# Optimization experiments

Hardware: AMD Instinct MI355X
Metric: run time of the kernel (lower is better)

## Reference

```python
import jax, jax.numpy as jnp
import numpy as np

S, LC = 8192, 16
CE = CH = 64      # char embed == char hidden (original quirk)
WE, HW = 128, 256 # word embed, word hidden
WV, CV, TAGS = 50000, 128, 50


def _lstm_step(h, c, x, Wih, Whh, bih, bhh):
    # PyTorch LSTM gate order: i, f, g, o
    g = x @ Wih.T + h @ Whh.T + bih + bhh
    i, f, gg, o = jnp.split(g, 4, axis=-1)
    c = jax.nn.sigmoid(f) * c + jax.nn.sigmoid(i) * jnp.tanh(gg)
    h = jax.nn.sigmoid(o) * jnp.tanh(c)
    return h, c


def setup_inputs() -> dict:
    key = jax.random.key(0)
    ks = jax.random.split(key, 16)
    inp = {
        'word_idxs': jax.random.randint(ks[0], (S,), 0, WV),
        'char_idxs': jax.random.randint(ks[1], (S, LC), 0, CV),
        'char_lens': jax.random.randint(ks[2], (S,), 1, LC + 1),
        'char_emb': jax.random.normal(ks[3], (CV, CE), jnp.float32) * 0.1,
        'char_Wih': jax.random.normal(ks[4], (4 * CH, CE), jnp.float32) * 0.1,
        'char_Whh': jax.random.normal(ks[5], (4 * CH, CH), jnp.float32) * 0.1,
        'char_bih': jax.random.normal(ks[6], (4 * CH,), jnp.float32) * 0.1,
        'char_bhh': jax.random.normal(ks[7], (4 * CH,), jnp.float32) * 0.1,
        'word_emb': jax.random.normal(ks[8], (WV, WE), jnp.float32) * 0.1,
        'word_Wih': jax.random.normal(ks[9], (4 * HW, WE + CH), jnp.float32) * 0.1,
        'word_Whh': jax.random.normal(ks[10], (4 * HW, HW), jnp.float32) * 0.1,
        'word_bih': jax.random.normal(ks[11], (4 * HW,), jnp.float32) * 0.1,
        'word_bhh': jax.random.normal(ks[12], (4 * HW,), jnp.float32) * 0.1,
        'tag_W': jax.random.normal(ks[13], (TAGS, HW), jnp.float32) * 0.1,
        'tag_b': jax.random.normal(ks[14], (TAGS,), jnp.float32) * 0.1,
    }
    return inp


def reference(word_idxs, char_idxs, char_lens,
              char_emb, char_Wih, char_Whh, char_bih, char_bhh,
              word_emb, word_Wih, word_Whh, word_bih, word_bhh,
              tag_W, tag_b):
    # --- char LSTM over all words in parallel (one fused scan over char time) ---
    cx = char_emb[char_idxs]                      # [S, LC, CE]
    cx = jnp.transpose(cx, (1, 0, 2))             # [LC, S, CE]

    def cstep(carry, x_t):
        h, c = carry
        h, c = _lstm_step(h, c, x_t, char_Wih, char_Whh, char_bih, char_bhh)
        return (h, c), h

    h0 = jnp.zeros((S, CH), cx.dtype)
    (_, _), hs = jax.lax.scan(cstep, (h0, h0), cx)  # hs: [LC, S, CH]
    # original takes char_lstm_out[-1] == hidden at position len(chars)-1
    char_feat = hs[char_lens - 1, jnp.arange(S)]    # [S, CH]

    # --- word LSTM over the sentence (batch = 1) ---
    wx = jnp.concatenate([word_emb[word_idxs], char_feat], axis=-1)  # [S, WE+CH]

    def wstep(carry, x_t):
        h, c = carry
        h, c = _lstm_step(h, c, x_t, word_Wih, word_Whh, word_bih, word_bhh)
        return (h, c), h

    wh0 = jnp.zeros((HW,), wx.dtype)
    (_, _), outs = jax.lax.scan(wstep, (wh0, wh0), wx)  # [S, HW]

    logits = outs @ tag_W.T + tag_b                     # [S, TAGS]
    return jax.nn.log_softmax(logits, axis=-1)
```

## Files before the change

### kernel.cpp

```cpp
#include <hip/hip_runtime.h>
#include <hip/hip_bf16.h>

#define S_LEN 8192
#define LC 16
#define CE 64
#define CH 64
#define WE 128
#define NTAGS 50

using bf16 = __hip_bfloat16;
typedef unsigned int u32;
typedef unsigned long long u64;

__device__ __forceinline__ float bfbits2f(unsigned short u) {
    union { unsigned int i; float f; } v; v.i = ((unsigned int)u) << 16; return v.f;
}
__device__ __forceinline__ float sigm(float x) {
    return __builtin_amdgcn_rcpf(1.0f + __expf(-x));
}
__device__ __forceinline__ float tanh_fast(float x) {
    return 1.0f - 2.0f * __builtin_amdgcn_rcpf(__expf(2.0f * x) + 1.0f);
}

template <bool BF>
__device__ __forceinline__ float ld1(const void* p, size_t i) {
    if constexpr (BF) return bfbits2f(((const unsigned short*)p)[i]);
    else              return ((const float*)p)[i];
}
template <bool BF>
__device__ __forceinline__ float4 ld4(const void* p, size_t i) {
    if constexpr (BF) {
        const ushort4 s = *reinterpret_cast<const ushort4*>((const unsigned short*)p + i);
        return make_float4(bfbits2f(s.x), bfbits2f(s.y), bfbits2f(s.z), bfbits2f(s.w));
    } else {
        return *reinterpret_cast<const float4*>((const float*)p + i);
    }
}
template <bool BF>
__device__ __forceinline__ void st1(void* p, size_t i, float v) {
    if constexpr (BF) ((bf16*)p)[i] = __float2bfloat16(v);
    else              ((float*)p)[i] = v;
}

__global__ void kdetect(const void* emb, u32* flag) {
    const int j = threadIdx.x;
    int s = 0;
    #pragma unroll
    for (int k = 0; k < 4; ++k) {
        const unsigned short u = ((const unsigned short*)emb)[j * 4 + k];
        const int e = (u >> 7) & 0xFF;
        s += (e >= 100 && e <= 133) ? 1 : 0;
    }
    #pragma unroll
    for (int off = 32; off >= 1; off >>= 1) s += __shfl_xor(s, off, 64);
    if (j == 0) *flag = (s >= 200) ? 1u : 0u;
}

template <bool BF>
__global__ __launch_bounds__(256, 2) void kchar(
        const u32* __restrict__ dtf,
        const int* __restrict__ char_idxs, const int* __restrict__ char_lens,
        const void* __restrict__ char_emb,
        const void* __restrict__ Wih, const void* __restrict__ Whh,
        const void* __restrict__ bih, const void* __restrict__ bhh,
        float* __restrict__ cfeat) {
    if ((*dtf != 0u) != BF) return;
    const int j = threadIdx.x;
    const int w0 = blockIdx.x * 8;

    __shared__ __align__(16) float emb_lds[128 * CE];
    __shared__ __align__(16) float gates_lds[8 * 256];
    __shared__ __align__(16) float h_lds[8 * CH];
    __shared__ __align__(16) float c_lds[8 * CH];
    __shared__ int cidx_lds[8 * LC];
    __shared__ int len_lds[8];

    {
        float4* emb4 = reinterpret_cast<float4*>(emb_lds);
        #pragma unroll
        for (int i = 0; i < 8; ++i) {
            const int c = i * 256 + j;
            emb4[c] = ld4<BF>(char_emb, (size_t)c * 4);
        }
    }
    if (j < 128) cidx_lds[j] = char_idxs[w0 * LC + j];
    if (j < 8)   len_lds[j]  = char_lens[w0 + j];
    h_lds[j] = 0.f; h_lds[j + 256] = 0.f;
    c_lds[j] = 0.f; c_lds[j + 256] = 0.f;

    float4 wih4[16], whh4[16];
    #pragma unroll
    for (int kc = 0; kc < 16; ++kc) {
        wih4[kc] = ld4<BF>(Wih, (size_t)j * CE + kc * 4);
        whh4[kc] = ld4<BF>(Whh, (size_t)j * CH + kc * 4);
    }
    const float bias = ld1<BF>(bih, j) + ld1<BF>(bhh, j);
    __syncthreads();

    for (int t = 0; t < LC; ++t) {
        for (int w = 0; w < 8; ++w) {
            const int ci = cidx_lds[w * LC + t];
            const float4* x4  = reinterpret_cast<const float4*>(emb_lds + ci * CE);
            const float4* hh4 = reinterpret_cast<const float4*>(h_lds + w * CH);
            float a0 = 0.f, a1 = 0.f, a2 = 0.f, a3 = 0.f;
            #pragma unroll
            for (int kc = 0; kc < 16; ++kc) {
                const float4 xv = x4[kc]; const float4 hv = hh4[kc];
                const float4 wi = wih4[kc]; const float4 wh = whh4[kc];
                a0 = fmaf(wi.x, xv.x, a0); a1 = fmaf(wi.y, xv.y, a1);
                a2 = fmaf(wi.z, xv.z, a2); a3 = fmaf(wi.w, xv.w, a3);
                a0 = fmaf(wh.x, hv.x, a0); a1 = fmaf(wh.y, hv.y, a1);
                a2 = fmaf(wh.z, hv.z, a2); a3 = fmaf(wh.w, hv.w, a3);
            }
            gates_lds[w * 256 + j] = bias + ((a0 + a1) + (a2 + a3));
        }
        __syncthreads();
        #pragma unroll
        for (int rep = 0; rep < 2; ++rep) {
            const int p = j + rep * 256;
            const int w = p >> 6, u = p & 63;
            const float ig = gates_lds[w * 256 + u];
            const float fg = gates_lds[w * 256 + 64 + u];
            const float gg = gates_lds[w * 256 + 128 + u];
            const float og = gates_lds[w * 256 + 192 + u];
            const float cn = sigm(fg) * c_lds[p] + sigm(ig) * tanh_fast(gg);
            const float hn = sigm(og) * tanh_fast(cn);
            c_lds[p] = cn; h_lds[p] = hn;
            if (t == len_lds[w] - 1)
                cfeat[(size_t)(w0 + w) * CH + u] = hn;
        }
        __syncthreads();
    }
}

template <bool BF>
__global__ __launch_bounds__(256) void kgx(
        const u32* __restrict__ dtf,
        int t0, const int* __restrict__ word_idxs, const float* __restrict__ cfeat,
        const void* __restrict__ wemb, const void* __restrict__ Wih,
        const void* __restrict__ bih, const void* __restrict__ bhh,
        float* __restrict__ Gxr) {
    if ((*dtf != 0u) != BF) return;
    const int j = threadIdx.x;
    const int wr0 = blockIdx.x * 16;
    const int w0g = t0 + wr0;
    __shared__ __align__(16) float wx[16 * 192];
    __shared__ int widx[16];
    if (j < 16) widx[j] = word_idxs[w0g + j];
    __syncthreads();
    {
        const int w = j >> 4, ch = j & 15;
        const size_t eb = (size_t)widx[w] * WE + ch * 8;
        const float4 f0 = ld4<BF>(wemb, eb), f1 = ld4<BF>(wemb, eb + 4);
        float4* dst = reinterpret_cast<float4*>(wx + w * 192 + ch * 8);
        dst[0] = f0; dst[1] = f1;
        const float4 cf = *reinterpret_cast<const float4*>(
            cfeat + (size_t)(w0g + w) * CH + ch * 4);
        *reinterpret_cast<float4*>(wx + w * 192 + WE + ch * 4) = cf;
    }
    __syncthreads();

    for (int g = 0; g < 4; ++g) {
        const int r = g * 256 + j;
        float acc[16];
        #pragma unroll
        for (int w = 0; w < 16; ++w) acc[w] = 0.f;
        #pragma unroll 8
        for (int kc = 0; kc < 48; ++kc) {
            const float4 wv = ld4<BF>(Wih, (size_t)r * 192 + kc * 4);
            #pragma unroll
            for (int w = 0; w < 16; ++w) {
                const float4 xv = *reinterpret_cast<const float4*>(wx + w * 192 + kc * 4);
                acc[w] = fmaf(wv.x, xv.x, acc[w]);
                acc[w] = fmaf(wv.y, xv.y, acc[w]);
                acc[w] = fmaf(wv.z, xv.z, acc[w]);
                acc[w] = fmaf(wv.w, xv.w, acc[w]);
            }
        }
        const float bias = ld1<BF>(bih, r) + ld1<BF>(bhh, r);
        #pragma unroll
        for (int w = 0; w < 16; ++w)
            Gxr[(size_t)(wr0 + w) * 1024 + r] = acc[w] + bias;
    }
}

template <bool BF>
__global__ __launch_bounds__(1024, 4) void kwlstm(
        const u32* __restrict__ dtf,
        int t0, int t1, int epoch, const void* __restrict__ whh,
        const float* __restrict__ Gxr,
        float* __restrict__ hallr, u64* hgx2, float* csave, u32* xccpub) {
    if ((*dtf != 0u) != BF) return;
    const int j = threadIdx.x;

    __shared__ int role_s;
    const u32 etag = 0xB0u + ((u32)epoch & 0xFu);
    if (j == 0) {
        const u32 xcc = __builtin_amdgcn_s_getreg(6164) & 0xFu;
        __hip_atomic_store(&xccpub[blockIdx.x], (etag << 24) | xcc,
                           __ATOMIC_RELAXED, __HIP_MEMORY_SCOPE_AGENT);
    }
    if (j < 64) {
        u32 v;
        do {
            v = __hip_atomic_load(&xccpub[j], __ATOMIC_RELAXED,
                                  __HIP_MEMORY_SCOPE_AGENT);
        } while ((v >> 24) != etag);
        const u32 v0 = __shfl(v, 0, 64);
        const u64 mask = __ballot((v & 0xFu) == (v0 & 0xFu));
        const int myb = blockIdx.x;
        int role = -1;
        if (__popcll(mask) >= 4) {
            if ((mask >> myb) & 1ull) {
                const int rank = __popcll(mask & ((1ull << myb) - 1ull));
                if (rank < 4) role = rank;
            }
        } else {
            if (myb < 4) role = myb;
        }
        if (j == 0) role_s = role;
    }
    __syncthreads();
    const int b = role_s;
    if (b < 0) return;

    const int r  = j & 255;
    const int kq = j >> 8;
    const int R  = ((r >> 6) << 8) + b * 64 + (r & 63);

    __shared__ __align__(16) float h_cur[256];
    __shared__ __align__(16) float part[1024];

    float4 wv[16];
    #pragma unroll
    for (int kc = 0; kc < 16; ++kc)
        wv[kc] = ld4<BF>(whh, (size_t)R * 256 + kq * 64 + kc * 4);

    if (j < 256) h_cur[j] = 0.f;
    float c_reg = 0.f;
    if (t0 > 0 && j < 64) c_reg = csave[b * 64 + j];

    float gxA = (j < 256) ? Gxr[(size_t)0 * 1024 + R] : 0.f;
    float gxB = (j < 256 && t0 + 1 < t1) ? Gxr[(size_t)1 * 1024 + R] : 0.f;
    __syncthreads();

    for (int t = t0; t < t1; ++t) {
        if (t > 0) {
            if (t == t0) {
                if (j < 256) {
                    u64 pk;
                    do {
                        pk = __hip_atomic_load(&hgx2[(size_t)(t & 1) * 256 + j],
                                               __ATOMIC_RELAXED, __HIP_MEMORY_SCOPE_AGENT);
                    } while ((u32)(pk >> 32) != (u32)t);
                    h_cur[j] = __uint_as_float((u32)pk);
                }
            } else {
                if (j < 192) {
                    const int gu = j + (j >= b * 64 ? 64 : 0);
                    u64 pk;
                    do {
                        pk = __hip_atomic_load(&hgx2[(size_t)(t & 1) * 256 + gu],
                                               __ATOMIC_RELAXED, __HIP_MEMORY_SCOPE_AGENT);
                    } while ((u32)(pk >> 32) != (u32)t);
                    h_cur[gu] = __uint_as_float((u32)pk);
                }
            }
        }
        __syncthreads();
        float gxN = 0.f;
        if (j < 256 && t + 2 < t1)
            gxN = Gxr[(size_t)(t + 2 - t0) * 1024 + R];
        float a0 = 0.f, a1 = 0.f, a2 = 0.f, a3 = 0.f;
        const float4* h4 = reinterpret_cast<const float4*>(h_cur) + kq * 16;
        #pragma unroll
        for (int kc = 0; kc < 16; ++kc) {
            const float4 hv = h4[kc];
            a0 = fmaf(wv[kc].x, hv.x, a0);
            a1 = fmaf(wv[kc].y, hv.y, a1);
            a2 = fmaf(wv[kc].z, hv.z, a2);
            a3 = fmaf(wv[kc].w, hv.w, a3);
        }
        part[j] = ((a0 + a1) + (a2 + a3)) + (kq == 0 ? gxA : 0.f);
        __syncthreads();
        if (j < 64) {
            const float ig = part[j]       + part[j + 256] + part[j + 512] + part[j + 768];
            const float fg = part[j + 64]  + part[j + 320] + part[j + 576] + part[j + 832];
            const float gg = part[j + 128] + part[j + 384] + part[j + 640] + part[j + 896];
            const float og = part[j + 192] + part[j + 448] + part[j + 704] + part[j + 960];
            const float cn = sigm(fg) * c_reg + sigm(ig) * tanh_fast(gg);
            c_reg = cn;
            const float hn = sigm(og) * tanh_fast(cn);
            const u64 pk = ((u64)(u32)(t + 1) << 32) | (u64)__float_as_uint(hn);
            __hip_atomic_store(&hgx2[(size_t)((t + 1) & 1) * 256 + b * 64 + j], pk,
                               __ATOMIC_RELAXED, __HIP_MEMORY_SCOPE_AGENT);
            h_cur[b * 64 + j] = hn;
            hallr[(size_t)(t - t0) * 256 + b * 64 + j] = hn;
        }
        gxA = gxB; gxB = gxN;
    }
    if (j < 64) csave[b * 64 + j] = c_reg;
}

template <bool BF>
__global__ __launch_bounds__(64) void ktag(
        const u32* __restrict__ dtf,
        int t0, const float* __restrict__ hallr, const void* __restrict__ tagW,
        const void* __restrict__ tagb, void* __restrict__ out) {
    if ((*dtf != 0u) != BF) return;
    const int tr = blockIdx.x, j = threadIdx.x;
    const int t = t0 + tr;
    __shared__ __align__(16) float4 h4[64];
    h4[j] = reinterpret_cast<const float4*>(hallr + (size_t)tr * 256)[j];
    __syncthreads();
    float logit = -1e30f;
    if (j < NTAGS) {
        float a0 = 0.f, a1 = 0.f, a2 = 0.f, a3 = 0.f;
        #pragma unroll
        for (int kc = 0; kc < 64; ++kc) {
            const float4 wvv = ld4<BF>(tagW, (size_t)j * 256 + kc * 4);
            const float4 hv = h4[kc];
            a0 = fmaf(wvv.x, hv.x, a0); a1 = fmaf(wvv.y, hv.y, a1);
            a2 = fmaf(wvv.z, hv.z, a2); a3 = fmaf(wvv.w, hv.w, a3);
        }
        logit = ld1<BF>(tagb, j) + ((a0 + a1) + (a2 + a3));
    }
    float m = logit;
    #pragma unroll
    for (int off = 32; off >= 1; off >>= 1) m = fmaxf(m, __shfl_xor(m, off, 64));
    const float e = (j < NTAGS) ? __expf(logit - m) : 0.f;
    float ssum = e;
    #pragma unroll
    for (int off = 32; off >= 1; off >>= 1) ssum += __shfl_xor(ssum, off, 64);
    if (j < NTAGS)
        st1<BF>(out, (size_t)t * NTAGS + j, logit - m - __logf(ssum));
}

extern "C" void kernel_launch(void* const* d_in, const int* in_sizes, int n_in,
                              void* d_out, int out_size, void* d_ws, size_t ws_size,
                              hipStream_t stream) {
    const int*  word_idxs = (const int*)d_in[0];
    const int*  char_idxs = (const int*)d_in[1];
    const int*  char_lens = (const int*)d_in[2];
    const void* char_emb  = d_in[3];
    const void* char_Wih  = d_in[4];
    const void* char_Whh  = d_in[5];
    const void* char_bih  = d_in[6];
    const void* char_bhh  = d_in[7];
    const void* word_emb  = d_in[8];
    const void* word_Wih  = d_in[9];
    const void* word_Whh  = d_in[10];
    const void* word_bih  = d_in[11];
    const void* word_bhh  = d_in[12];
    const void* tag_W     = d_in[13];
    const void* tag_b     = d_in[14];

    char* ws = (char*)d_ws;
    u32*   dtf    = (u32*)(ws);
    u64*   hgx2   = (u64*)(ws + 64);
    float* csave  = (float*)(ws + 4224);
    u32*   xccpub = (u32*)(ws + 5248);
    float* cfeat  = (float*)(ws + 8192);
    const size_t ring0 = 8192 + (size_t)S_LEN * CH * 4;

    int NC = 256;
    const int ncs[9] = {1, 2, 4, 8, 16, 32, 64, 128, 256};
    for (int i = 0; i < 9; ++i) {
        const int ct = S_LEN / ncs[i];
        if (ring0 + (size_t)ct * 5120 <= ws_size) { NC = ncs[i]; break; }
    }
    const int CT = S_LEN / NC;
    float* Gxr   = (float*)(ws + ring0);
    float* hallr = (float*)(ws + ring0 + (size_t)CT * 4096);

    hipLaunchKernelGGL(kdetect, dim3(1), dim3(64), 0, stream, char_emb, dtf);
    hipLaunchKernelGGL(kchar<true>,  dim3(S_LEN / 8), dim3(256), 0, stream,
                       dtf, char_idxs, char_lens, char_emb, char_Wih, char_Whh,
                       char_bih, char_bhh, cfeat);
    hipLaunchKernelGGL(kchar<false>, dim3(S_LEN / 8), dim3(256), 0, stream,
                       dtf, char_idxs, char_lens, char_emb, char_Wih, char_Whh,
                       char_bih, char_bhh, cfeat);
    for (int c = 0; c < NC; ++c) {
        const int t0 = c * CT;
        hipLaunchKernelGGL(kgx<true>,  dim3(CT / 16), dim3(256), 0, stream,
                           dtf, t0, word_idxs, cfeat, word_emb, word_Wih,
                           word_bih, word_bhh, Gxr);
        hipLaunchKernelGGL(kgx<false>, dim3(CT / 16), dim3(256), 0, stream,
                           dtf, t0, word_idxs, cfeat, word_emb, word_Wih,
                           word_bih, word_bhh, Gxr);
        hipLaunchKernelGGL(kwlstm<true>,  dim3(64), dim3(1024), 0, stream,
                           dtf, t0, t0 + CT, c, word_Whh, Gxr, hallr, hgx2, csave, xccpub);
        hipLaunchKernelGGL(kwlstm<false>, dim3(64), dim3(1024), 0, stream,
                           dtf, t0, t0 + CT, c, word_Whh, Gxr, hallr, hgx2, csave, xccpub);
        hipLaunchKernelGGL(ktag<true>,  dim3(CT), dim3(64), 0, stream,
                           dtf, t0, hallr, tag_W, tag_b, d_out);
        hipLaunchKernelGGL(ktag<false>, dim3(CT), dim3(64), 0, stream,
                           dtf, t0, hallr, tag_W, tag_b, d_out);
    }
}
```

Before: 12.18 ms.

## Replace per-step block barriers with tagged LDS flags and windowed gate staging

Restructures the word-LSTM recurrence so the 16 waves of each block each poll the global h exchange directly for their own 64-element slice. They publish partial dot products through tagged LDS slots, and wave 0 spins on those slots instead of using two __syncthreads per timestep. Input gate projections are staged in LDS 32 steps at a time, and h outputs are buffered and written back per window. This removes the block-wide barriers on the serial critical path, at the cost of heavier spin traffic on the global flags and the assumption that step counts are multiples of 32.

```diff
diff --git a/kernel.cpp b/kernel.cpp
--- a/kernel.cpp
+++ b/kernel.cpp
@@ -224,82 +224,117 @@
     const int b = role_s;
     if (b < 0) return;
 
-    const int r  = j & 255;
-    const int kq = j >> 8;
-    const int R  = ((r >> 6) << 8) + b * 64 + (r & 63);
-
-    __shared__ __align__(16) float h_cur[256];
-    __shared__ __align__(16) float part[1024];
+    const int w  = j >> 6;
+    const int l  = j & 63;
+    const int kq = w >> 2;
+    const int g  = w & 3;
+    const int R  = g * 256 + b * 64 + l;
+    const int kbase = kq * 64;
+
+    __shared__ __align__(16) float hsl[16][64];
+    __shared__ __align__(16) u64 partp[2][16][64];
+    __shared__ __align__(16) float gxw[32][4][64];
+    __shared__ __align__(16) float hwin[32][64];
 
     float4 wv[16];
     #pragma unroll
     for (int kc = 0; kc < 16; ++kc)
-        wv[kc] = ld4<BF>(whh, (size_t)R * 256 + kq * 64 + kc * 4);
-
-    if (j < 256) h_cur[j] = 0.f;
+        wv[kc] = ld4<BF>(whh, (size_t)R * 256 + kbase + kc * 4);
+
+    {
+        u64* pz = &partp[0][0][0];
+        pz[j] = 0ull; pz[j + 1024] = 0ull;
+    }
     float c_reg = 0.f;
-    if (t0 > 0 && j < 64) c_reg = csave[b * 64 + j];
-
-    float gxA = (j < 256) ? Gxr[(size_t)0 * 1024 + R] : 0.f;
-    float gxB = (j < 256 && t0 + 1 < t1) ? Gxr[(size_t)1 * 1024 + R] : 0.f;
-    __syncthreads();
-
-    for (int t = t0; t < t1; ++t) {
-        if (t > 0) {
-            if (t == t0) {
-                if (j < 256) {
-                    u64 pk;
+    if (w == 0 && t0 > 0) c_reg = csave[b * 64 + l];
+    __syncthreads();
+
+    for (int tw = t0; tw < t1; tw += 32) {
+        __syncthreads();
+        if (tw > t0) {
+            #pragma unroll
+            for (int k = 0; k < 2; ++k) {
+                const int flat = j + k * 1024;
+                const int s = flat >> 6, u = flat & 63;
+                hallr[(size_t)(tw - 32 - t0 + s) * 256 + b * 64 + u] = hwin[s][u];
+            }
+        }
+        #pragma unroll
+        for (int k = 0; k < 8; ++k) {
+            const int flat = j + k * 1024;
+            const int s = flat >> 8, rem = flat & 255;
+            const int gg = rem >> 6, u = rem & 63;
+            gxw[s][gg][u] =
+                Gxr[(size_t)(tw - t0 + s) * 1024 + gg * 256 + b * 64 + u];
+        }
+        __syncthreads();
+
+        for (int s = 0; s < 32; ++s) {
+            const int t = tw + s;
+            const int par = t & 1;
+            const u32 ptag = (u32)(t - t0 + 1);
+            if (t == 0) {
+                hsl[w][l] = 0.f;
+            } else {
+                u64 pk;
+                do {
+                    pk = __hip_atomic_load(&hgx2[(size_t)par * 256 + kbase + l],
+                                           __ATOMIC_RELAXED, __HIP_MEMORY_SCOPE_AGENT);
+                } while ((u32)(pk >> 32) != (u32)t);
+                hsl[w][l] = __uint_as_float((u32)pk);
+            }
+            float a0 = 0.f, a1 = 0.f, a2 = 0.f, a3 = 0.f;
+            const float4* h4 = reinterpret_cast<const float4*>(&hsl[w][0]);
+            #pragma unroll
+            for (int kc = 0; kc < 16; ++kc) {
+                const float4 hv = h4[kc];
+                a0 = fmaf(wv[kc].x, hv.x, a0);
+                a1 = fmaf(wv[kc].y, hv.y, a1);
+                a2 = fmaf(wv[kc].z, hv.z, a2);
+                a3 = fmaf(wv[kc].w, hv.w, a3);
+            }
+            const float psum = (a0 + a1) + (a2 + a3);
+            if (w != 0) {
+                const u64 pp = ((u64)ptag << 32) | (u64)__float_as_uint(psum);
+                __hip_atomic_store(&partp[par][w][l], pp, __ATOMIC_RELAXED,
+                                   __HIP_MEMORY_SCOPE_WORKGROUP);
+            } else {
+                float acc0 = psum + gxw[s][0][l];
+                float acc1 = gxw[s][1][l];
+                float acc2 = gxw[s][2][l];
+                float acc3 = gxw[s][3][l];
+                #pragma unroll
+                for (int ww = 1; ww < 16; ++ww) {
+                    u64 pp;
                     do {
-                        pk = __hip_atomic_load(&hgx2[(size_t)(t & 1) * 256 + j],
-                                               __ATOMIC_RELAXED, __HIP_MEMORY_SCOPE_AGENT);
-                    } while ((u32)(pk >> 32) != (u32)t);
-                    h_cur[j] = __uint_as_float((u32)pk);
+                        pp = __hip_atomic_load(&partp[par][ww][l], __ATOMIC_RELAXED,
+                                               __HIP_MEMORY_SCOPE_WORKGROUP);
+                    } while ((u32)(pp >> 32) != ptag);
+                    const float pv = __uint_as_float((u32)pp);
+                    const int gg = ww & 3;
+                    if (gg == 0) acc0 += pv;
+                    else if (gg == 1) acc1 += pv;
+                    else if (gg == 2) acc2 += pv;
+                    else acc3 += pv;
                 }
-            } else {
-                if (j < 192) {
-                    const int gu = j + (j >= b * 64 ? 64 : 0);
-                    u64 pk;
-                    do {
-                        pk = __hip_atomic_load(&hgx2[(size_t)(t & 1) * 256 + gu],
-                                               __ATOMIC_RELAXED, __HIP_MEMORY_SCOPE_AGENT);
-                    } while ((u32)(pk >> 32) != (u32)t);
-                    h_cur[gu] = __uint_as_float((u32)pk);
-                }
-            }
-        }
-        __syncthreads();
-        float gxN = 0.f;
-        if (j < 256 && t + 2 < t1)
-            gxN = Gxr[(size_t)(t + 2 - t0) * 1024 + R];
-        float a0 = 0.f, a1 = 0.f, a2 = 0.f, a3 = 0.f;
-        const float4* h4 = reinterpret_cast<const float4*>(h_cur) + kq * 16;
-        #pragma unroll
-        for (int kc = 0; kc < 16; ++kc) {
-            const float4 hv = h4[kc];
-            a0 = fmaf(wv[kc].x, hv.x, a0);
-            a1 = fmaf(wv[kc].y, hv.y, a1);
-            a2 = fmaf(wv[kc].z, hv.z, a2);
-            a3 = fmaf(wv[kc].w, hv.w, a3);
-        }
-        part[j] = ((a0 + a1) + (a2 + a3)) + (kq == 0 ? gxA : 0.f);
-        __syncthreads();
-        if (j < 64) {
-            const float ig = part[j]       + part[j + 256] + part[j + 512] + part[j + 768];
-            const float fg = part[j + 64]  + part[j + 320] + part[j + 576] + part[j + 832];
-            const float gg = part[j + 128] + part[j + 384] + part[j + 640] + part[j + 896];
-            const float og = part[j + 192] + part[j + 448] + part[j + 704] + part[j + 960];
-            const float cn = sigm(fg) * c_reg + sigm(ig) * tanh_fast(gg);
-            c_reg = cn;
-            const float hn = sigm(og) * tanh_fast(cn);
-            const u64 pk = ((u64)(u32)(t + 1) << 32) | (u64)__float_as_uint(hn);
-            __hip_atomic_store(&hgx2[(size_t)((t + 1) & 1) * 256 + b * 64 + j], pk,
-                               __ATOMIC_RELAXED, __HIP_MEMORY_SCOPE_AGENT);
-            h_cur[b * 64 + j] = hn;
-            hallr[(size_t)(t - t0) * 256 + b * 64 + j] = hn;
-        }
-        gxA = gxB; gxB = gxN;
-    }
-    if (j < 64) csave[b * 64 + j] = c_reg;
+                const float cn = sigm(acc1) * c_reg + sigm(acc0) * tanh_fast(acc2);
+                c_reg = cn;
+                const float hn = sigm(acc3) * tanh_fast(cn);
+                hwin[s][l] = hn;
+                const u64 pk = ((u64)(u32)(t + 1) << 32) | (u64)__float_as_uint(hn);
+                __hip_atomic_store(&hgx2[(size_t)((t + 1) & 1) * 256 + b * 64 + l],
+                                   pk, __ATOMIC_RELAXED, __HIP_MEMORY_SCOPE_AGENT);
+            }
+        }
+    }
+    __syncthreads();
+    #pragma unroll
+    for (int k = 0; k < 2; ++k) {
+        const int flat = j + k * 1024;
+        const int s = flat >> 6, u = flat & 63;
+        hallr[(size_t)(t1 - 32 - t0 + s) * 256 + b * 64 + u] = hwin[s][u];
+    }
+    if (w == 0) csave[b * 64 + l] = c_reg;
 }
 
 template <bool BF>
```

New measurement: 17.56 ms. 1.44x slower.
